# Optimization experiments

Measured on AMD Instinct MI355X. Metric: run time of the kernel, lower is better.

## Reference

```python
import jax, jax.numpy as jnp
import numpy as np

K_POS, K_NEG = 3, 2
MIN_D = 9  # min_dist=8 bumped to next odd, as in _nms_topk
BN_EPS = 1e-5


def _conv(x, w, pad):
    return jax.lax.conv_general_dilated(
        x, w, (1, 1), [(pad, pad), (pad, pad)],
        dimension_numbers=('NCHW', 'OIHW', 'NCHW'))


def _bn(x, g, b, m, v):
    scale = g * jax.lax.rsqrt(v + BN_EPS)  # inference-mode BN
    return x * scale[None, :, None, None] + (b - m * scale)[None, :, None, None]


def _head(x, w1, g1, b1, m1, v1, w2, g2, b2, m2, v2, w3, b3, out_hw):
    h = jax.nn.relu(_bn(_conv(x, w1, 1), g1, b1, m1, v1))
    h = jax.nn.relu(_bn(_conv(h, w2, 1), g2, b2, m2, v2))
    logits = _conv(h, w3, 0) + b3[None, :, None, None]
    B = logits.shape[0]
    # F.interpolate(mode='bilinear', align_corners=False) == half-pixel bilinear resize
    logits = jax.image.resize(logits, (B, 1, out_hw, out_hw), method='bilinear')
    return logits


def _sample_one(smap, key):
    # smap: [H, W] sigmoid heatmap for one sample
    H, W = smap.shape
    # --- positive points: NMS-style peak top-k ---
    local_max = jax.lax.reduce_window(
        smap, -jnp.inf, jax.lax.max, (MIN_D, MIN_D), (1, 1), 'SAME')
    is_peak = (smap == local_max) & (smap > 0.1)
    masked = jnp.where(is_peak, smap, -jnp.inf).reshape(-1)
    vals, idx = jax.lax.top_k(masked, K_POS)
    valid = jnp.isfinite(vals)  # slots corresponding to real peaks
    xs = jnp.where(valid, (idx % W).astype(jnp.float32), 0.0)
    ys = jnp.where(valid, (idx // W).astype(jnp.float32), 0.0)
    pos_lab = jnp.where(valid, 1, -1).astype(jnp.int32)
    # fallback: no peak at all -> single argmax point in slot 0
    amax = jnp.argmax(smap)
    any_peak = valid[0]
    xs = xs.at[0].set(jnp.where(any_peak, xs[0], (amax % W).astype(jnp.float32)))
    ys = ys.at[0].set(jnp.where(any_peak, ys[0], (amax // W).astype(jnp.float32)))
    pos_lab = pos_lab.at[0].set(1)  # slot 0 is always a positive point
    pos = jnp.stack([xs, ys], axis=1)  # [K_POS, 2] (x, y)
    # --- negative points: uniform sample from low-response region ---
    low = (smap < 0.3).reshape(-1)
    low_fb = (smap < smap.max()).reshape(-1)
    mask = jnp.where(jnp.any(low), low, low_fb)
    n = mask.sum()
    # stable argsort puts masked-in (True) flat indices first, in index order
    order = jnp.argsort(jnp.logical_not(mask))
    u = jax.random.uniform(key, (K_NEG,))
    ridx = jnp.minimum((u * jnp.maximum(n, 1).astype(jnp.float32)).astype(jnp.int32),
                       jnp.maximum(n - 1, 0))
    sel = order[ridx]
    neg = jnp.stack([sel % W, sel // W], axis=1).astype(jnp.float32)
    neg = jnp.where(n > 0, neg, jnp.zeros_like(neg))
    neg_lab = jnp.zeros((K_NEG,), jnp.int32)
    coords = jnp.concatenate([pos, neg], axis=0)      # [K_POS+K_NEG, 2]
    labels = jnp.concatenate([pos_lab, neg_lab], axis=0)
    return coords, labels


def setup_inputs() -> dict:
    key = jax.random.key(0)
    ks = jax.random.split(key, 4)
    B, C, h, w = 32, 256, 64, 64
    HID = 64
    x = jax.random.normal(ks[0], (B, C, h, w), jnp.float32)
    w1 = jax.random.normal(ks[1], (HID, C, 3, 3), jnp.float32) * 0.03  # kaiming-ish
    w2 = jax.random.normal(ks[2], (HID, HID, 3, 3), jnp.float32) * 0.06
    w3 = jax.random.normal(ks[3], (1, HID, 1, 1), jnp.float32) * 0.17
    b3 = jnp.full((1,), -2.0, jnp.float32)
    ones = jnp.ones((HID,), jnp.float32)
    zeros = jnp.zeros((HID,), jnp.float32)
    return {
        'encoder_features': x,
        'w1': w1, 'g1': ones, 'b1': zeros, 'm1': zeros, 'v1': ones,
        'w2': w2, 'g2': ones, 'b2': zeros, 'm2': zeros, 'v2': ones,
        'w3': w3, 'b3': b3,
        'output_size': 256,
    }


def reference(encoder_features, w1, g1, b1, m1, v1, w2, g2, b2, m2, v2, w3, b3, output_size):
    logits = _head(encoder_features, w1, g1, b1, m1, v1, w2, g2, b2, m2, v2, w3, b3, output_size)
    heatmap = jax.nn.sigmoid(logits)  # [B, 1, H, W]
    B = heatmap.shape[0]
    keys = jax.random.split(jax.random.key(42), B)
    coords, labels = jax.vmap(_sample_one)(heatmap[:, 0], keys)
    point_coords = coords[:, None].astype(jnp.float32)  # [B, 1, K, 2]
    point_labels = labels[:, None].astype(jnp.int32)    # [B, 1, K]
    return heatmap, point_coords, point_labels, logits
```

## Files before the change

### kernel.cpp

```cpp
#include <hip/hip_runtime.h>
#include <stdint.h>
#include <math.h>

#define NEG_INF (-__builtin_inff())
#define IDX_SENT 0x7fffffff

typedef __attribute__((address_space(1))) const void gas_t;
typedef __attribute__((address_space(3))) void las_t;

__device__ __forceinline__ void threefry2x32(uint32_t k0, uint32_t k1,
                                             uint32_t x0, uint32_t x1,
                                             uint32_t* o0, uint32_t* o1) {
  const uint32_t ks2 = k0 ^ k1 ^ 0x1BD11BDAu;
  uint32_t ks[3] = {k0, k1, ks2};
  const int rot[2][4] = {{13, 15, 26, 6}, {17, 29, 16, 24}};
  x0 += ks[0];
  x1 += ks[1];
#pragma unroll
  for (int i = 0; i < 5; ++i) {
#pragma unroll
    for (int j = 0; j < 4; ++j) {
      const int r = rot[i & 1][j];
      x0 += x1;
      x1 = (x1 << r) | (x1 >> (32 - r));
      x1 ^= x0;
    }
    x0 += ks[(i + 1) % 3];
    x1 += ks[(i + 2) % 3] + (uint32_t)(i + 1);
  }
  *o0 = x0;
  *o1 = x1;
}

__device__ __forceinline__ float bits_to_uniform(uint32_t bits) {
  return __uint_as_float((bits >> 9) | 0x3f800000u) - 1.0f;
}

__device__ __forceinline__ void top3_insert(float v, int idx, float tv[3], int ti[3]) {
  if ((v > tv[2]) || (v == tv[2] && idx < ti[2])) {
    tv[2] = v; ti[2] = idx;
    if ((tv[2] > tv[1]) || (tv[2] == tv[1] && ti[2] < ti[1])) {
      float fv = tv[1]; int fi = ti[1];
      tv[1] = tv[2]; ti[1] = ti[2];
      tv[2] = fv;     ti[2] = fi;
      if ((tv[1] > tv[0]) || (tv[1] == tv[0] && ti[1] < ti[0])) {
        fv = tv[0]; fi = ti[0];
        tv[0] = tv[1]; ti[0] = ti[1];
        tv[1] = fv;    ti[1] = fi;
      }
    }
  }
}

__global__ __launch_bounds__(256) void transpose_w4(
    const float* __restrict__ w, float* __restrict__ wt, int IC9) {
  const int idx = blockIdx.x * 256 + threadIdx.x;
  const int qrow = idx >> 6;
  const int oc = idx & 63;
  const float4 v = *(const float4*)&w[(size_t)oc * IC9 + qrow * 4];
  wt[(size_t)(qrow * 4 + 0) * 64 + oc] = v.x;
  wt[(size_t)(qrow * 4 + 1) * 64 + oc] = v.y;
  wt[(size_t)(qrow * 4 + 2) * 64 + oc] = v.z;
  wt[(size_t)(qrow * 4 + 3) * 64 + oc] = v.w;
}

template <int IC>
__global__ __launch_bounds__(512, 3) void conv3x3_bn_relu(
    const float* __restrict__ x, const float* __restrict__ wt,
    const float* __restrict__ g, const float* __restrict__ bb,
    const float* __restrict__ m, const float* __restrict__ vv,
    float* __restrict__ out) {
  __shared__ float xs[2][8][10][36];

  const int tid = threadIdx.x;
  const int blk = blockIdx.x;
  const int ocg = blk >> 9;
  const int b = (blk >> 4) & 31;
  const int tile = blk & 15;
  const int by = (tile >> 1) << 3;
  const int bx = (tile & 1) << 5;
  const int wv = __builtin_amdgcn_readfirstlane(tid >> 6);
  const int lane = tid & 63;
  const int rh = wv & 1;
  const int os = wv >> 1;
  const int r = (lane & 3) | (rh << 2);
  const int lc = (lane >> 2) << 1;
  const int ocbase = (ocg << 5) | (os << 3);

  const int sc = lane;
  const int gx = bx + sc - 1;
  const bool cok = (sc < 34) && (gx >= 0) && (gx < 64);

  float acc[2][8];
#pragma unroll
  for (int p = 0; p < 2; ++p)
#pragma unroll
    for (int o = 0; o < 8; ++o) acc[p][o] = 0.0f;

  for (int l = tid; l < 2 * 8 * 10 * 36; l += 512)
    (&xs[0][0][0][0])[l] = 0.0f;
  __syncthreads();

  auto stage = [&](int buf, int icb0) {
    if (cok) {
      const float* gb = x + ((size_t)b * IC + icb0 + wv) * 4096 + (by - 1) * 64 + gx;
#pragma unroll
      for (int rr = 0; rr < 10; ++rr) {
        const int gy = by + rr - 1;
        if (gy >= 0 && gy < 64) {
          __builtin_amdgcn_global_load_lds(
              (gas_t*)(const void*)(gb + rr * 64),
              (las_t*)(void*)(&xs[buf][wv][rr][0]),
              4, 0, 0);
        }
      }
    }
  };

  stage(0, 0);
  __syncthreads();

  int cur = 0;
  for (int icb = 0; icb < IC; icb += 8) {
    if (icb + 8 < IC) stage(cur ^ 1, icb + 8);

    const float* wbase = wt + (size_t)icb * 9 * 64 + ocbase;
    for (int ic = 0; ic < 8; ++ic) {
#pragma unroll
      for (int ky = 0; ky < 3; ++ky) {
        float xv[4];
        *(float2*)&xv[0] = *(const float2*)&xs[cur][ic][r + ky][lc];
        *(float2*)&xv[2] = *(const float2*)&xs[cur][ic][r + ky][lc + 2];
#pragma unroll
        for (int kx = 0; kx < 3; ++kx) {
          const float4* wp4 = (const float4*)(wbase + (ic * 9 + ky * 3 + kx) * 64);
#pragma unroll
          for (int q = 0; q < 2; ++q) {
            const float4 w4 = wp4[q];
#pragma unroll
            for (int p = 0; p < 2; ++p) {
              acc[p][4 * q + 0] = fmaf(xv[kx + p], w4.x, acc[p][4 * q + 0]);
              acc[p][4 * q + 1] = fmaf(xv[kx + p], w4.y, acc[p][4 * q + 1]);
              acc[p][4 * q + 2] = fmaf(xv[kx + p], w4.z, acc[p][4 * q + 2]);
              acc[p][4 * q + 3] = fmaf(xv[kx + p], w4.w, acc[p][4 * q + 3]);
            }
          }
        }
      }
    }
    __syncthreads();
    cur ^= 1;
  }

#pragma unroll
  for (int o = 0; o < 8; ++o) {
    const int oc = ocbase + o;
    const float sc2 = g[oc] * (1.0f / sqrtf(vv[oc] + 1e-5f));
    const float sh = bb[oc] - m[oc] * sc2;
    float2 v;
    v.x = fmaxf(fmaf(acc[0][o], sc2, sh), 0.0f);
    v.y = fmaxf(fmaf(acc[1][o], sc2, sh), 0.0f);
    *(float2*)&out[(((size_t)b * 64 + oc) * 64 + (by + r)) * 64 + bx + lc] = v;
  }
}

__global__ __launch_bounds__(256) void logits64_k(
    const float* __restrict__ h2, const float* __restrict__ w3,
    const float* __restrict__ b3, float* __restrict__ lg64) {
  const int blk = blockIdx.x;
  const int b = blk >> 4;
  const int p = ((blk & 15) << 8) + threadIdx.x;
  __shared__ float wvv[64];
  if (threadIdx.x < 64) wvv[threadIdx.x] = w3[threadIdx.x];
  __syncthreads();
  float s = b3[0];
  const float* hp = h2 + (size_t)b * 64 * 4096 + p;
  for (int oc = 0; oc < 64; ++oc)
    s = fmaf(hp[(size_t)oc * 4096], wvv[oc], s);
  lg64[b * 4096 + p] = s;
}

__global__ __launch_bounds__(256) void upsample_k(
    const float* __restrict__ lg64, float* __restrict__ logits,
    float* __restrict__ heat) {
  const int blk = blockIdx.x;
  const int b = blk >> 6;
  const int qq = ((blk & 63) << 10) + (threadIdx.x << 2);
  const float* lg = lg64 + b * 4096;
  const int oy = qq >> 8;
  const float sy = (float)oy * 0.25f - 0.375f;
  const float fy = floorf(sy);
  const int y0 = (int)fy;
  const float ty = sy - fy;
  const int y0c = y0 < 0 ? 0 : y0;
  const int y1c = (y0 + 1) > 63 ? 63 : (y0 + 1);
  const float* r0 = lg + y0c * 64;
  const float* r1 = lg + y1c * 64;
  float4 lo, he;
  float* lop = (float*)&lo;
  float* hep = (float*)&he;
#pragma unroll
  for (int j = 0; j < 4; ++j) {
    const int ox = (qq & 255) + j;
    const float sx = (float)ox * 0.25f - 0.375f;
    const float fx = floorf(sx);
    const int x0 = (int)fx;
    const float tx = sx - fx;
    const int x0c = x0 < 0 ? 0 : x0;
    const int x1c = (x0 + 1) > 63 ? 63 : (x0 + 1);
    const float v00 = r0[x0c], v01 = r0[x1c];
    const float v10 = r1[x0c], v11 = r1[x1c];
    const float vtop = v00 + (v01 - v00) * tx;
    const float vbot = v10 + (v11 - v10) * tx;
    const float val = vtop + (vbot - vtop) * ty;
    lop[j] = val;
    hep[j] = 1.0f / (1.0f + expf(-val));
  }
  const size_t o = (size_t)b * 65536 + qq;
  *(float4*)(logits + o) = lo;
  *(float4*)(heat + o) = he;
}

__global__ __launch_bounds__(256) void pos_stripe(
    const float* __restrict__ heat, float* __restrict__ cand) {
  const int b = blockIdx.x >> 4;
  const int stripe = blockIdx.x & 15;
  const int y0 = stripe << 4;
  const float* s = heat + (size_t)b * 65536;
  const int tid = threadIdx.x;
  __shared__ float sm[24][256];
  __shared__ float rm[24][256];
  __shared__ float rv[256 * 3];
  __shared__ int ri[256 * 3];
  __shared__ float mvv[256];
  __shared__ int mii[256];
  __shared__ float rv2[24];
  __shared__ int ri2[24];
  __shared__ float mv2[8];
  __shared__ int mi2[8];

  for (int l = tid; l < 24 * 256; l += 256) {
    const int rr = l >> 8, xx = l & 255;
    const int gy = y0 - 4 + rr;
    sm[rr][xx] = (gy >= 0 && gy < 256) ? s[gy * 256 + xx] : NEG_INF;
  }
  __syncthreads();
  for (int l = tid; l < 24 * 256; l += 256) {
    const int rr = l >> 8, xx = l & 255;
    const int lo = (xx - 4 < 0) ? 0 : xx - 4;
    const int hi = (xx + 4 > 255) ? 255 : xx + 4;
    float mx = NEG_INF;
    for (int x2 = lo; x2 <= hi; ++x2) mx = fmaxf(mx, sm[rr][x2]);
    rm[rr][xx] = mx;
  }
  __syncthreads();

  float tv[3] = {NEG_INF, NEG_INF, NEG_INF};
  int ti[3] = {IDX_SENT, IDX_SENT, IDX_SENT};
  float bmax = NEG_INF;
  int bidx = IDX_SENT;
  for (int l = tid; l < 16 * 256; l += 256) {
    const int ry = l >> 8, xx = l & 255;
    const int lr = ry + 4;
    const float v = sm[lr][xx];
    float lm = rm[lr - 4][xx];
#pragma unroll
    for (int d = -3; d <= 4; ++d) lm = fmaxf(lm, rm[lr + d][xx]);
    const int gidx = (y0 + ry) * 256 + xx;
    if (v > bmax) { bmax = v; bidx = gidx; }
    if (v == lm && v > 0.1f) top3_insert(v, gidx, tv, ti);
  }

  rv[tid * 3 + 0] = tv[0]; rv[tid * 3 + 1] = tv[1]; rv[tid * 3 + 2] = tv[2];
  ri[tid * 3 + 0] = ti[0]; ri[tid * 3 + 1] = ti[1]; ri[tid * 3 + 2] = ti[2];
  mvv[tid] = bmax; mii[tid] = bidx;
  __syncthreads();

  if (tid < 8) {
    float av[3] = {NEG_INF, NEG_INF, NEG_INF};
    int ai[3] = {IDX_SENT, IDX_SENT, IDX_SENT};
    float am = NEG_INF; int amI = IDX_SENT;
    for (int t = tid * 32; t < tid * 32 + 32; ++t) {
      for (int k = 0; k < 3; ++k) top3_insert(rv[t * 3 + k], ri[t * 3 + k], av, ai);
      if (mvv[t] > am || (mvv[t] == am && mii[t] < amI)) { am = mvv[t]; amI = mii[t]; }
    }
    rv2[tid * 3 + 0] = av[0]; rv2[tid * 3 + 1] = av[1]; rv2[tid * 3 + 2] = av[2];
    ri2[tid * 3 + 0] = ai[0]; ri2[tid * 3 + 1] = ai[1]; ri2[tid * 3 + 2] = ai[2];
    mv2[tid] = am; mi2[tid] = amI;
  }
  __syncthreads();

  if (tid == 0) {
    float fv[3] = {NEG_INF, NEG_INF, NEG_INF};
    int fi[3] = {IDX_SENT, IDX_SENT, IDX_SENT};
    for (int t = 0; t < 24; ++t) top3_insert(rv2[t], ri2[t], fv, fi);
    float gbv = NEG_INF; int gbi = IDX_SENT;
    for (int t = 0; t < 8; ++t)
      if (mv2[t] > gbv || (mv2[t] == gbv && mi2[t] < gbi)) { gbv = mv2[t]; gbi = mi2[t]; }
    float* c = cand + ((size_t)b * 16 + stripe) * 8;
    c[0] = fv[0]; c[1] = __int_as_float(fi[0]);
    c[2] = fv[1]; c[3] = __int_as_float(fi[1]);
    c[4] = fv[2]; c[5] = __int_as_float(fi[2]);
    c[6] = gbv;   c[7] = __int_as_float(gbi);
  }
}

__global__ void pos_final(const float* __restrict__ cand,
                          float* __restrict__ coords, float* __restrict__ labels) {
  const int b = blockIdx.x;
  if (threadIdx.x != 0) return;
  float fv[3] = {NEG_INF, NEG_INF, NEG_INF};
  int fi[3] = {IDX_SENT, IDX_SENT, IDX_SENT};
  float gbv = NEG_INF; int gbi = IDX_SENT;
  for (int st = 0; st < 16; ++st) {
    const float* c = cand + ((size_t)b * 16 + st) * 8;
    for (int k = 0; k < 3; ++k)
      top3_insert(c[2 * k], __float_as_int(c[2 * k + 1]), fv, fi);
    const float mv = c[6]; const int mi = __float_as_int(c[7]);
    if (mv > gbv || (mv == gbv && mi < gbi)) { gbv = mv; gbi = mi; }
  }
  float* co = coords + (size_t)b * 10;
  float* la = labels + (size_t)b * 5;
  const bool any_peak = (fi[0] != IDX_SENT);
  const int i0 = any_peak ? fi[0] : gbi;
  co[0] = (float)(i0 & 255);
  co[1] = (float)(i0 >> 8);
  la[0] = 1.0f;
  for (int k = 1; k < 3; ++k) {
    const bool valid = (fi[k] != IDX_SENT);
    co[k * 2 + 0] = valid ? (float)(fi[k] & 255) : 0.0f;
    co[k * 2 + 1] = valid ? (float)(fi[k] >> 8) : 0.0f;
    la[k] = valid ? 1.0f : -1.0f;
  }
}

__global__ __launch_bounds__(256) void neg_count(
    const float* __restrict__ heat, float* __restrict__ ncnt,
    float* __restrict__ pmax) {
  const int blk = blockIdx.x;
  const int b = blk >> 2;
  const int part = blk & 3;
  const int tid = threadIdx.x;
  const int chunk = (part << 8) + tid;
  const float4* s = (const float4*)(heat + (size_t)b * 65536 + chunk * 64);
  int c = 0;
  float mx = NEG_INF;
  for (int i = 0; i < 16; ++i) {
    const float4 v = s[i];
    c += (v.x < 0.3f) + (v.y < 0.3f) + (v.z < 0.3f) + (v.w < 0.3f);
    mx = fmaxf(mx, fmaxf(fmaxf(v.x, v.y), fmaxf(v.z, v.w)));
  }
  ncnt[b * 1024 + chunk] = (float)c;
  __shared__ float mxs[256];
  mxs[tid] = mx;
  __syncthreads();
  if (tid == 0) {
    float gmx = NEG_INF;
    for (int t = 0; t < 256; ++t) gmx = fmaxf(gmx, mxs[t]);
    pmax[blk] = gmx;
  }
}

__global__ __launch_bounds__(256) void neg_select(
    const float* __restrict__ heat, const float* __restrict__ ncnt,
    const float* __restrict__ pmax, float* __restrict__ coords,
    float* __restrict__ labels) {
  const int b = blockIdx.x;
  const int tid = threadIdx.x;
  const float* s = heat + (size_t)b * 65536;
  __shared__ float cnt[1024];
  __shared__ float c256[256];
  __shared__ int pfx[257];
  __shared__ float thr_s;
  __shared__ int fb_s;
  __shared__ int n_s;
  __shared__ int ridx_s[2];

  for (int l = tid; l < 1024; l += 256) cnt[l] = ncnt[b * 1024 + l];
  __syncthreads();
  c256[tid] = cnt[4 * tid] + cnt[4 * tid + 1] + cnt[4 * tid + 2] + cnt[4 * tid + 3];
  __syncthreads();
  if (tid == 0) {
    int tot = 0;
    for (int t = 0; t < 256; ++t) tot += (int)c256[t];
    const float gm = fmaxf(fmaxf(pmax[b * 4], pmax[b * 4 + 1]),
                           fmaxf(pmax[b * 4 + 2], pmax[b * 4 + 3]));
    fb_s = (tot > 0) ? 0 : 1;
    thr_s = (tot > 0) ? 0.3f : gm;
  }
  __syncthreads();
  if (fb_s) {
    const float t2 = thr_s;
    const int base = tid * 256;
    int c = 0;
    for (int i = 0; i < 256; ++i) c += (s[base + i] < t2) ? 1 : 0;
    c256[tid] = (float)c;
    __syncthreads();
  }
  if (tid == 0) {
    int run = 0;
    for (int t = 0; t < 256; ++t) { pfx[t] = run; run += (int)c256[t]; }
    pfx[256] = run;
    const int n = run;
    n_s = n;
    uint32_t k0, k1, a0, a1;
    threefry2x32(0u, 42u, 0u, (uint32_t)b, &k0, &k1);
    threefry2x32(k0, k1, 0u, 0u, &a0, &a1);
    const uint32_t bits0 = a0 ^ a1;
    threefry2x32(k0, k1, 0u, 1u, &a0, &a1);
    const uint32_t bits1 = a0 ^ a1;
    const float u0 = bits_to_uniform(bits0);
    const float u1 = bits_to_uniform(bits1);
    const float nf = (float)(n > 1 ? n : 1);
    int r0 = (int)(u0 * nf);
    int r1 = (int)(u1 * nf);
    const int rmax = (n - 1 > 0) ? n - 1 : 0;
    ridx_s[0] = r0 < rmax ? r0 : rmax;
    ridx_s[1] = r1 < rmax ? r1 : rmax;
    labels[(size_t)b * 5 + 3] = 0.0f;
    labels[(size_t)b * 5 + 4] = 0.0f;
    if (n == 0) {
      coords[(size_t)b * 10 + 6] = 0.0f; coords[(size_t)b * 10 + 7] = 0.0f;
      coords[(size_t)b * 10 + 8] = 0.0f; coords[(size_t)b * 10 + 9] = 0.0f;
    }
  }
  __syncthreads();
  const int n = n_s;
  if (n > 0) {
    const float t2 = thr_s;
    const int p0 = pfx[tid], p1 = pfx[tid + 1];
    const int base = tid * 256;
    for (int j = 0; j < 2; ++j) {
      const int r = ridx_s[j];
      if (r >= p0 && r < p1) {
        int need = r - p0;
        int sel = -1;
        for (int i = 0; i < 256; ++i) {
          if (s[base + i] < t2) {
            if (need == 0) { sel = base + i; break; }
            --need;
          }
        }
        coords[(size_t)b * 10 + 6 + j * 2 + 0] = (float)(sel & 255);
        coords[(size_t)b * 10 + 6 + j * 2 + 1] = (float)(sel >> 8);
      }
    }
  }
}

extern "C" void kernel_launch(void* const* d_in, const int* in_sizes, int n_in,
                              void* d_out, int out_size, void* d_ws, size_t ws_size,
                              hipStream_t stream) {
  (void)in_sizes; (void)n_in; (void)out_size; (void)ws_size;
  const float* x  = (const float*)d_in[0];
  const float* w1 = (const float*)d_in[1];
  const float* g1 = (const float*)d_in[2];
  const float* b1 = (const float*)d_in[3];
  const float* m1 = (const float*)d_in[4];
  const float* v1 = (const float*)d_in[5];
  const float* w2 = (const float*)d_in[6];
  const float* g2 = (const float*)d_in[7];
  const float* b2 = (const float*)d_in[8];
  const float* m2 = (const float*)d_in[9];
  const float* v2 = (const float*)d_in[10];
  const float* w3 = (const float*)d_in[11];
  const float* b3 = (const float*)d_in[12];

  float* out = (float*)d_out;
  float* heat = out;
  float* coords = out + (size_t)32 * 65536;
  float* labels = coords + 320;
  float* logits = labels + 160;

  float* w1t = logits;
  float* w2t = logits + 147456;

  float* h1 = (float*)d_ws;
  float* h2 = h1 + (size_t)32 * 64 * 64 * 64;
  float* lg64 = h1;
  float* cand = h1 + 131072;
  float* ncnt = h1 + 135168;
  float* pmax = h1 + 167936;

  transpose_w4<<<144, 256, 0, stream>>>(w1, w1t, 2304);
  transpose_w4<<<36, 256, 0, stream>>>(w2, w2t, 576);
  conv3x3_bn_relu<256><<<1024, 512, 0, stream>>>(x, w1t, g1, b1, m1, v1, h1);
  conv3x3_bn_relu<64><<<1024, 512, 0, stream>>>(h1, w2t, g2, b2, m2, v2, h2);
  logits64_k<<<512, 256, 0, stream>>>(h2, w3, b3, lg64);
  upsample_k<<<2048, 256, 0, stream>>>(lg64, logits, heat);
  pos_stripe<<<512, 256, 0, stream>>>(heat, cand);
  pos_final<<<32, 64, 0, stream>>>(cand, coords, labels);
  neg_count<<<128, 256, 0, stream>>>(heat, ncnt, pmax);
  neg_select<<<32, 256, 0, stream>>>(heat, ncnt, pmax, coords, labels);
}
```

Measured before the change: 830.8 us.

## Enlarge conv per-thread tile to 4x8 and software-pipeline LDS/weight loads

Each block now covers all 64 output channels, with each thread computing 4 pixels by 8 channels instead of 2x8. The grid is halved and the input tile staged in LDS is reused across twice as many output channels. The inner loop is rewritten with double-buffered register loads (A/B ping-pong) so the loads for the next (ic,ky) row overlap the FMAs of the current one. This raises register pressure, with 32 accumulators plus 12 float4 weight registers under launch_bounds(512,3), and halves the number of blocks, which lowers parallelism on a large GPU.

```diff
diff --git a/kernel.cpp b/kernel.cpp
--- a/kernel.cpp
+++ b/kernel.cpp
@@ -74,26 +74,23 @@
 
   const int tid = threadIdx.x;
   const int blk = blockIdx.x;
-  const int ocg = blk >> 9;
-  const int b = (blk >> 4) & 31;
+  const int b = blk >> 4;
   const int tile = blk & 15;
   const int by = (tile >> 1) << 3;
   const int bx = (tile & 1) << 5;
   const int wv = __builtin_amdgcn_readfirstlane(tid >> 6);
   const int lane = tid & 63;
-  const int rh = wv & 1;
-  const int os = wv >> 1;
-  const int r = (lane & 3) | (rh << 2);
-  const int lc = (lane >> 2) << 1;
-  const int ocbase = (ocg << 5) | (os << 3);
+  const int r = lane & 7;
+  const int lc = (lane >> 3) << 2;
+  const int ocbase = wv << 3;
 
   const int sc = lane;
   const int gx = bx + sc - 1;
   const bool cok = (sc < 34) && (gx >= 0) && (gx < 64);
 
-  float acc[2][8];
-#pragma unroll
-  for (int p = 0; p < 2; ++p)
+  float acc[4][8];
+#pragma unroll
+  for (int p = 0; p < 4; ++p)
 #pragma unroll
     for (int o = 0; o < 8; ++o) acc[p][o] = 0.0f;
 
@@ -125,29 +122,46 @@
     if (icb + 8 < IC) stage(cur ^ 1, icb + 8);
 
     const float* wbase = wt + (size_t)icb * 9 * 64 + ocbase;
-    for (int ic = 0; ic < 8; ++ic) {
-#pragma unroll
-      for (int ky = 0; ky < 3; ++ky) {
-        float xv[4];
-        *(float2*)&xv[0] = *(const float2*)&xs[cur][ic][r + ky][lc];
-        *(float2*)&xv[2] = *(const float2*)&xs[cur][ic][r + ky][lc + 2];
-#pragma unroll
-        for (int kx = 0; kx < 3; ++kx) {
-          const float4* wp4 = (const float4*)(wbase + (ic * 9 + ky * 3 + kx) * 64);
-#pragma unroll
-          for (int q = 0; q < 2; ++q) {
-            const float4 w4 = wp4[q];
-#pragma unroll
-            for (int p = 0; p < 2; ++p) {
-              acc[p][4 * q + 0] = fmaf(xv[kx + p], w4.x, acc[p][4 * q + 0]);
-              acc[p][4 * q + 1] = fmaf(xv[kx + p], w4.y, acc[p][4 * q + 1]);
-              acc[p][4 * q + 2] = fmaf(xv[kx + p], w4.z, acc[p][4 * q + 2]);
-              acc[p][4 * q + 3] = fmaf(xv[kx + p], w4.w, acc[p][4 * q + 3]);
-            }
+
+    float xvA[6], xvB[6];
+    float4 wA[6], wB[6];
+
+    auto loadu = [&](float* xv, float4* w, int ic, int ky) {
+      *(float4*)&xv[0] = *(const float4*)&xs[cur][ic][r + ky][lc];
+      *(float2*)&xv[4] = *(const float2*)&xs[cur][ic][r + ky][lc + 4];
+      const float4* wp = (const float4*)(wbase + (ic * 9 + ky * 3) * 64);
+      w[0] = wp[0];  w[1] = wp[1];
+      w[2] = wp[16]; w[3] = wp[17];
+      w[4] = wp[32]; w[5] = wp[33];
+    };
+    auto compute = [&](const float* xv, const float4* w) {
+#pragma unroll
+      for (int kx = 0; kx < 3; ++kx)
+#pragma unroll
+        for (int q = 0; q < 2; ++q) {
+          const float4 w4 = w[kx * 2 + q];
+#pragma unroll
+          for (int p = 0; p < 4; ++p) {
+            acc[p][4 * q + 0] = fmaf(xv[kx + p], w4.x, acc[p][4 * q + 0]);
+            acc[p][4 * q + 1] = fmaf(xv[kx + p], w4.y, acc[p][4 * q + 1]);
+            acc[p][4 * q + 2] = fmaf(xv[kx + p], w4.z, acc[p][4 * q + 2]);
+            acc[p][4 * q + 3] = fmaf(xv[kx + p], w4.w, acc[p][4 * q + 3]);
           }
         }
-      }
-    }
+    };
+
+    loadu(xvA, wA, 0, 0);
+    for (int ic2 = 0; ic2 < 4; ++ic2) {
+      const int ic0 = ic2 * 2;
+      loadu(xvB, wB, ic0, 1);       compute(xvA, wA);
+      loadu(xvA, wA, ic0, 2);       compute(xvB, wB);
+      loadu(xvB, wB, ic0 + 1, 0);   compute(xvA, wA);
+      loadu(xvA, wA, ic0 + 1, 1);   compute(xvB, wB);
+      loadu(xvB, wB, ic0 + 1, 2);   compute(xvA, wA);
+      if (ic2 < 3) loadu(xvA, wA, ic0 + 2, 0);
+      compute(xvB, wB);
+    }
+
     __syncthreads();
     cur ^= 1;
   }
@@ -157,10 +171,12 @@
     const int oc = ocbase + o;
     const float sc2 = g[oc] * (1.0f / sqrtf(vv[oc] + 1e-5f));
     const float sh = bb[oc] - m[oc] * sc2;
-    float2 v;
+    float4 v;
     v.x = fmaxf(fmaf(acc[0][o], sc2, sh), 0.0f);
     v.y = fmaxf(fmaf(acc[1][o], sc2, sh), 0.0f);
-    *(float2*)&out[(((size_t)b * 64 + oc) * 64 + (by + r)) * 64 + bx + lc] = v;
+    v.z = fmaxf(fmaf(acc[2][o], sc2, sh), 0.0f);
+    v.w = fmaxf(fmaf(acc[3][o], sc2, sh), 0.0f);
+    *(float4*)&out[(((size_t)b * 64 + oc) * 64 + (by + r)) * 64 + bx + lc] = v;
   }
 }
 
@@ -484,8 +500,8 @@
 
   transpose_w4<<<144, 256, 0, stream>>>(w1, w1t, 2304);
   transpose_w4<<<36, 256, 0, stream>>>(w2, w2t, 576);
-  conv3x3_bn_relu<256><<<1024, 512, 0, stream>>>(x, w1t, g1, b1, m1, v1, h1);
-  conv3x3_bn_relu<64><<<1024, 512, 0, stream>>>(h1, w2t, g2, b2, m2, v2, h2);
+  conv3x3_bn_relu<256><<<512, 512, 0, stream>>>(x, w1t, g1, b1, m1, v1, h1);
+  conv3x3_bn_relu<64><<<512, 512, 0, stream>>>(h1, w2t, g2, b2, m2, v2, h2);
   logits64_k<<<512, 256, 0, stream>>>(h2, w3, b3, lg64);
   upsample_k<<<2048, 256, 0, stream>>>(lg64, logits, heat);
   pos_stripe<<<512, 256, 0, stream>>>(heat, cand);
```

Measured after the change: 782.4 us. -5.8%, faster.
